# Performance work log

Hardware: AMD Instinct MI355X
Metric: run time of the kernel (lower is better)

## Reference

```python
import jax, jax.numpy as jnp
import numpy as np

EMBED = 512
HEADS = 8
INTER = 512
HEAD_DIM = INTER // HEADS
ROPE_BASE = 10000.0


def rot_half(x):
    x1 = x[..., ::2]
    x2 = x[..., 1::2]
    return jnp.stack([-x2, x1], axis=-1).reshape(x.shape)


def apply_rope(x, cos, sin):
    # cos/sin: (1, T, 1, 1, D//2) -> repeat-interleave to D
    cos = jnp.repeat(cos, 2, axis=-1)
    sin = jnp.repeat(sin, 2, axis=-1)
    return x * cos + rot_half(x) * sin


def setup_inputs() -> dict:
    key = jax.random.key(0)
    ks = jax.random.split(key, 8)
    B, T, P, E = 2, 512, 16, EMBED
    s_in = 1.0 / np.sqrt(E)
    x = jax.random.normal(ks[0], (B, T, P, E), dtype=jnp.float32)
    q_w = jax.random.normal(ks[1], (INTER, E), dtype=jnp.float32) * s_in
    k_w = jax.random.normal(ks[2], (INTER, E), dtype=jnp.float32) * s_in
    v_w = jax.random.normal(ks[3], (INTER, E), dtype=jnp.float32) * s_in
    q_b = jax.random.normal(ks[4], (INTER,), dtype=jnp.float32) * 0.01
    k_b = jax.random.normal(ks[5], (INTER,), dtype=jnp.float32) * 0.01
    v_b = jax.random.normal(ks[6], (INTER,), dtype=jnp.float32) * 0.01
    proj_w = jax.random.normal(ks[7], (E, INTER), dtype=jnp.float32) * (1.0 / np.sqrt(INTER))
    return {"x": x, "q_w": q_w, "q_b": q_b, "k_w": k_w, "k_b": k_b,
            "v_w": v_w, "v_b": v_b, "proj_w": proj_w}


def reference(x, q_w, q_b, k_w, k_b, v_w, v_b, proj_w):
    B, T, P, E = x.shape
    H, D = HEADS, HEAD_DIM
    q = (x @ q_w.T + q_b).reshape(B, T, P, H, D)
    k = (x @ k_w.T + k_b).reshape(B, T, P, H, D)
    v = (x @ v_w.T + v_b).reshape(B, T, P, H, D)
    # RoPE cache over time axis
    inv_freq = 1.0 / (ROPE_BASE ** (jnp.arange(0, D, 2, dtype=jnp.float32) / D))
    freqs = jnp.arange(T, dtype=jnp.float32)[:, None] * inv_freq[None, :]  # (T, D//2)
    cos_t = jnp.cos(freqs).reshape(1, T, 1, 1, D // 2)
    sin_t = jnp.sin(freqs).reshape(1, T, 1, 1, D // 2)
    q = apply_rope(q, cos_t, sin_t)
    k = apply_rope(k, cos_t, sin_t)
    scale = D ** (-0.5)
    scores = jnp.einsum('btphd,buphd->bphtu', q, k) * scale  # (B,P,H,T,T)
    causal_mask = jnp.triu(jnp.ones((T, T), dtype=bool), k=1)
    scores = jnp.where(causal_mask, -jnp.inf, scores)
    probs = jax.nn.softmax(scores, axis=-1)
    y = jnp.einsum('bphtu,buphd->btphd', probs, v).reshape(B, T, P, H * D)
    return y @ proj_w.T
```

## Files before the change

kernel.cpp:

```cpp
#include <hip/hip_runtime.h>
#include <hip/hip_bf16.h>
#include <math.h>

typedef __bf16 bf16x8 __attribute__((ext_vector_type(8)));
typedef float f32x4 __attribute__((ext_vector_type(4)));
typedef unsigned short u16;

#define MROWS 16384
#define TT 512
#define PP 16

__device__ __forceinline__ u16 f2bf(float f) {
    union { float f; unsigned int i; } v; v.f = f;
    unsigned int x = v.i;
    return (u16)((x + 0x7FFFu + ((x >> 16) & 1u)) >> 16);
}

__device__ __forceinline__ void async16(const u16* g, u16* lds) {
    __builtin_amdgcn_global_load_lds(
        (const __attribute__((address_space(1))) void*)g,
        (__attribute__((address_space(3))) void*)lds, 16, 0, 0);
}

__global__ __launch_bounds__(256) void cvt_k(const float* __restrict__ s,
                                             u16* __restrict__ d) {
    long i = (long)blockIdx.x * 256 + threadIdx.x;
    const float4* p = (const float4*)s + i * 2;
    float4 a = p[0], b = p[1];
    u16 t[8] = { f2bf(a.x), f2bf(a.y), f2bf(a.z), f2bf(a.w),
                 f2bf(b.x), f2bf(b.y), f2bf(b.z), f2bf(b.w) };
    *(uint4*)(d + i * 8) = *(const uint4*)t;
}

__global__ __launch_bounds__(256) void cvtw_k(const float* __restrict__ q,
                                              const float* __restrict__ k,
                                              const float* __restrict__ v,
                                              const float* __restrict__ pw,
                                              u16* __restrict__ d) {
    int m = blockIdx.y;
    const float* s = (m == 0) ? q : (m == 1) ? k : (m == 2) ? v : pw;
    long i = (long)blockIdx.x * 256 + threadIdx.x;
    const float4* p = (const float4*)s + i * 2;
    float4 a = p[0], b = p[1];
    u16 t[8] = { f2bf(a.x), f2bf(a.y), f2bf(a.z), f2bf(a.w),
                 f2bf(b.x), f2bf(b.y), f2bf(b.z), f2bf(b.w) };
    *(uint4*)(d + (long)m * 262144 + i * 8) = *(const uint4*)t;
}

template<bool QKV>
__global__ __launch_bounds__(256, 2)
void gemm_k(const u16* __restrict__ A, const u16* __restrict__ Wall,
            const float* __restrict__ bq, const float* __restrict__ bk,
            const float* __restrict__ bv,
            u16* __restrict__ Oq, u16* __restrict__ Ok, u16* __restrict__ Ov,
            float* __restrict__ Of)
{
    __shared__ u16 As[128 * 64];
    __shared__ u16 Bs[128 * 64];

    const int tid  = threadIdx.x;
    const int wv   = tid >> 6;
    const int lane = tid & 63;
    const int quad = lane >> 4;
    const int l16  = lane & 15;
    const int wm   = wv >> 1, wn = wv & 1;

    const int blockM = blockIdx.x;
    const int blockN = blockIdx.y;

    const u16* W; const float* bias; u16* OutB; int ncol0; int section = 0;
    if constexpr (QKV) {
        section = blockN >> 2;
        ncol0 = (blockN & 3) * 128;
        W    = Wall + (long)section * 262144;
        bias = (section == 0) ? bq : (section == 1) ? bk : bv;
        OutB = (section == 0) ? Oq : (section == 1) ? Ok : Ov;
    } else {
        ncol0 = blockN * 128;
        W = Wall; bias = nullptr; OutB = nullptr;
    }

    const int gm0 = blockM * 128;
    const int lr  = lane >> 3;
    const int lc  = (lane & 7) ^ lr;

    f32x4 acc[4][4] = {};

    for (int kk = 0; kk < 8; ++kk) {
        const int k0 = kk * 64;
        __syncthreads();
        #pragma unroll
        for (int i = 0; i < 4; ++i) {
            const int rb = wv * 32 + i * 8;
            async16(&A[(long)(gm0   + rb + lr) * 512 + k0 + lc * 8], &As[rb * 64]);
            async16(&W[(long)(ncol0 + rb + lr) * 512 + k0 + lc * 8], &Bs[rb * 64]);
        }
        __syncthreads();

        #pragma unroll
        for (int ks = 0; ks < 2; ++ks) {
            bf16x8 af[4], bf_[4];
            #pragma unroll
            for (int ms = 0; ms < 4; ++ms) {
                const int R = wm * 64 + ms * 16 + l16;
                af[ms] = *(const bf16x8*)&As[(R * 8 + ((ks * 4 + quad) ^ (l16 & 7))) * 8];
            }
            #pragma unroll
            for (int ns = 0; ns < 4; ++ns) {
                const int R = wn * 64 + ns * 16 + l16;
                bf_[ns] = *(const bf16x8*)&Bs[(R * 8 + ((ks * 4 + quad) ^ (l16 & 7))) * 8];
            }
            #pragma unroll
            for (int ms = 0; ms < 4; ++ms)
                #pragma unroll
                for (int ns = 0; ns < 4; ++ns)
                    acc[ms][ns] = __builtin_amdgcn_mfma_f32_16x16x32_bf16(af[ms], bf_[ns], acc[ms][ns], 0, 0, 0);
        }
    }

    #pragma unroll
    for (int ms = 0; ms < 4; ++ms) {
        const int g_m0 = gm0 + wm * 64 + ms * 16 + quad * 4;
        #pragma unroll
        for (int ns = 0; ns < 4; ++ns) {
            const int n_local = ncol0 + wn * 64 + ns * 16 + l16;
            float bval = 0.f;
            if constexpr (QKV) bval = bias[n_local];
            #pragma unroll
            for (int r = 0; r < 4; ++r) {
                float val = acc[ms][ns][r] + bval;
                const size_t off = (size_t)(g_m0 + r) * 512 + n_local;
                if constexpr (QKV) {
                    float partner = __shfl_xor(val, 1, 64);
                    if (section < 2) {
                        const int m = g_m0 + r;
                        const int t = (m >> 4) & 511;
                        const int d = n_local & 63;
                        float ang = (float)t * __expf(-(float)(d & ~1) * (9.210340371976184f / 64.0f));
                        float s_, c_;
                        __sincosf(ang, &s_, &c_);
                        val = (d & 1) ? (val * c_ + partner * s_)
                                      : (val * c_ - partner * s_);
                    }
                    OutB[off] = f2bf(val);
                } else {
                    Of[off] = val;
                }
            }
        }
    }
}

__global__ __launch_bounds__(256, 4)
void attn_k(const u16* __restrict__ Q, const u16* __restrict__ K,
            const u16* __restrict__ V, u16* __restrict__ Y)
{
    __shared__ u16 Sh[128][72];
    __shared__ u16 Vt[64][72];

    const int tid  = threadIdx.x;
    const int wv   = tid >> 6;
    const int lane = tid & 63;
    const int quad = lane >> 4;
    const int l16  = lane & 15;

    const int pairx = blockIdx.x;
    const int hid = blockIdx.y;
    const int b = hid >> 7;
    const int p = (hid >> 3) & 15;
    const int h = hid & 7;

    const int base = ((b * TT) * PP + p) * 512 + h * 64;
    const int rowStride = PP * 512;

    for (int sel = 0; sel < 2; ++sel) {
        const int qt = (sel == 0) ? pairx : 3 - pairx;
        const int t0 = qt * 128;

        __syncthreads();
        #pragma unroll
        for (int i = 0; i < 4; ++i) {
            int task = tid + i * 256;
            int row = task >> 3, c = (task & 7) * 8;
            *(uint4*)&Sh[row][c] = *(const uint4*)&Q[base + (t0 + row) * rowStride + c];
        }
        __syncthreads();
        bf16x8 qf[2][2];
        #pragma unroll
        for (int ms = 0; ms < 2; ++ms)
            #pragma unroll
            for (int ks = 0; ks < 2; ++ks)
                qf[ms][ks] = *(const bf16x8*)&Sh[wv*32 + ms*16 + l16][ks*32 + quad*8];

        float m_i[8], l_i[8], alpha[8];
        f32x4 o[2][4] = {};
        #pragma unroll
        for (int j = 0; j < 8; ++j) { m_i[j] = -3.0e38f; l_i[j] = 0.f; }

        const int nUT = (qt + 1) * 2;
        for (int ui = 0; ui < nUT; ++ui) {
            const int u0 = ui * 64;
            __syncthreads();
            #pragma unroll
            for (int i = 0; i < 2; ++i) {
                int task = tid + i * 256;
                int row = task >> 3, c = (task & 7) * 8;
                *(uint4*)&Sh[row][c] = *(const uint4*)&K[base + (u0 + row) * rowStride + c];
            }
            #pragma unroll
            for (int i = 0; i < 4; ++i) {
                int task = tid + i * 256;
                int u = task >> 4, dc = (task & 15) * 4;
                uint2 vvv = *(const uint2*)&V[base + (u0 + u) * rowStride + dc];
                Vt[dc + 0][u] = (u16)(vvv.x & 0xFFFF);
                Vt[dc + 1][u] = (u16)(vvv.x >> 16);
                Vt[dc + 2][u] = (u16)(vvv.y & 0xFFFF);
                Vt[dc + 3][u] = (u16)(vvv.y >> 16);
            }
            __syncthreads();

            f32x4 s[2][4] = {};
            #pragma unroll
            for (int ks = 0; ks < 2; ++ks) {
                bf16x8 bk_[4];
                #pragma unroll
                for (int ns = 0; ns < 4; ++ns)
                    bk_[ns] = *(const bf16x8*)&Sh[ns*16 + l16][ks*32 + quad*8];
                #pragma unroll
                for (int ms = 0; ms < 2; ++ms)
                    #pragma unroll
                    for (int ns = 0; ns < 4; ++ns)
                        s[ms][ns] = __builtin_amdgcn_mfma_f32_16x16x32_bf16(qf[ms][ks], bk_[ns], s[ms][ns], 0, 0, 0);
            }
            __syncthreads();

            #pragma unroll
            for (int ms = 0; ms < 2; ++ms)
                #pragma unroll
                for (int ns = 0; ns < 4; ++ns)
                    #pragma unroll
                    for (int r = 0; r < 4; ++r) {
                        int trow = t0 + wv*32 + ms*16 + quad*4 + r;
                        int ucol = u0 + ns*16 + l16;
                        float v = s[ms][ns][r] * 0.125f;
                        s[ms][ns][r] = (ucol > trow) ? -1.0e30f : v;
                    }
            #pragma unroll
            for (int ms = 0; ms < 2; ++ms) {
                #pragma unroll
                for (int r = 0; r < 4; ++r) {
                    const int j = ms*4 + r;
                    float tmax = s[ms][0][r];
                    #pragma unroll
                    for (int ns = 1; ns < 4; ++ns) tmax = fmaxf(tmax, s[ms][ns][r]);
                    #pragma unroll
                    for (int off = 1; off < 16; off <<= 1)
                        tmax = fmaxf(tmax, __shfl_xor(tmax, off, 64));
                    float mn = fmaxf(m_i[j], tmax);
                    alpha[j] = __expf(fminf(m_i[j] - mn, 0.f));
                    m_i[j] = mn;
                    float rsum = 0.f;
                    #pragma unroll
                    for (int ns = 0; ns < 4; ++ns) {
                        float e = __expf(fminf(s[ms][ns][r] - mn, 0.f));
                        s[ms][ns][r] = e;
                        rsum += e;
                    }
                    #pragma unroll
                    for (int off = 1; off < 16; off <<= 1)
                        rsum += __shfl_xor(rsum, off, 64);
                    l_i[j] = l_i[j] * alpha[j] + rsum;
                }
            }
            #pragma unroll
            for (int ms = 0; ms < 2; ++ms)
                #pragma unroll
                for (int nd = 0; nd < 4; ++nd)
                    #pragma unroll
                    for (int r = 0; r < 4; ++r)
                        o[ms][nd][r] *= alpha[ms*4 + r];
            #pragma unroll
            for (int ms = 0; ms < 2; ++ms)
                #pragma unroll
                for (int ns = 0; ns < 4; ++ns)
                    #pragma unroll
                    for (int r = 0; r < 4; ++r)
                        Sh[wv*32 + ms*16 + quad*4 + r][ns*16 + l16] = f2bf(s[ms][ns][r]);
            __syncthreads();
            #pragma unroll
            for (int ks = 0; ks < 2; ++ks) {
                bf16x8 ap[2], bv_[4];
                #pragma unroll
                for (int ms = 0; ms < 2; ++ms)
                    ap[ms] = *(const bf16x8*)&Sh[wv*32 + ms*16 + l16][ks*32 + quad*8];
                #pragma unroll
                for (int nd = 0; nd < 4; ++nd)
                    bv_[nd] = *(const bf16x8*)&Vt[nd*16 + l16][ks*32 + quad*8];
                #pragma unroll
                for (int ms = 0; ms < 2; ++ms)
                    #pragma unroll
                    for (int nd = 0; nd < 4; ++nd)
                        o[ms][nd] = __builtin_amdgcn_mfma_f32_16x16x32_bf16(ap[ms], bv_[nd], o[ms][nd], 0, 0, 0);
            }
        }

        #pragma unroll
        for (int ms = 0; ms < 2; ++ms)
            #pragma unroll
            for (int nd = 0; nd < 4; ++nd)
                #pragma unroll
                for (int r = 0; r < 4; ++r) {
                    int t = t0 + wv*32 + ms*16 + quad*4 + r;
                    int d = nd*16 + l16;
                    float val = o[ms][nd][r] / l_i[ms*4 + r];
                    int ym = (b * TT + t) * PP + p;
                    Y[ym * 512 + h * 64 + d] = f2bf(val);
                }
    }
}

extern "C" void kernel_launch(void* const* d_in, const int* in_sizes, int n_in,
                              void* d_out, int out_size, void* d_ws, size_t ws_size,
                              hipStream_t stream) {
    const float* x  = (const float*)d_in[0];
    const float* qw = (const float*)d_in[1];
    const float* qb = (const float*)d_in[2];
    const float* kw = (const float*)d_in[3];
    const float* kb = (const float*)d_in[4];
    const float* vw = (const float*)d_in[5];
    const float* vb = (const float*)d_in[6];
    const float* pw = (const float*)d_in[7];

    u16* ws   = (u16*)d_ws;
    u16* xb   = ws;
    u16* wAll = ws + (size_t)MROWS * 512;
    u16* Qb   = wAll + 4 * 262144;
    u16* Vb   = (u16*)d_out;
    u16* Kb   = (u16*)d_out + (size_t)MROWS * 512;

    cvt_k<<<4096, 256, 0, stream>>>(x, xb);
    cvtw_k<<<dim3(128, 4), 256, 0, stream>>>(qw, kw, vw, pw, wAll);
    gemm_k<true><<<dim3(128, 12), 256, 0, stream>>>(xb, wAll, qb, kb, vb,
                                                    Qb, Kb, Vb, nullptr);
    attn_k<<<dim3(2, 256), 256, 0, stream>>>(Qb, Kb, Vb, Qb);
    gemm_k<false><<<dim3(128, 4), 256, 0, stream>>>(Qb, wAll + 3 * 262144,
                                                    nullptr, nullptr, nullptr,
                                                    nullptr, nullptr, nullptr,
                                                    (float*)d_out);
}
```

Measured before the change: 227.7 us.

## Shrink attention query tile to 64 rows with swizzled async LDS loads

The attention kernel now handles 64-row query tiles instead of 128, pairing tiles (p, 7-p) so causal work stays balanced, and launches twice as many blocks. Q and K tiles go into an unpadded XOR-swizzled LDS buffer via async global-to-LDS loads, and the causal mask runs only on the diagonal tile. The aim is more parallelism and occupancy, less LDS, fewer masking ALU ops and no register staging for loads. In exchange each block reloads K/V more often relative to its MFMA work, since each wave now computes a single 16-row slice.

```diff
diff --git a/kernel.cpp b/kernel.cpp
--- a/kernel.cpp
+++ b/kernel.cpp
@@ -155,7 +155,7 @@
 void attn_k(const u16* __restrict__ Q, const u16* __restrict__ K,
             const u16* __restrict__ V, u16* __restrict__ Y)
 {
-    __shared__ u16 Sh[128][72];
+    __shared__ u16 Sh[64 * 64];
     __shared__ u16 Vt[64][72];
 
     const int tid  = threadIdx.x;
@@ -163,6 +163,8 @@
     const int lane = tid & 63;
     const int quad = lane >> 4;
     const int l16  = lane & 15;
+    const int lr   = lane >> 3;
+    const int lc   = (lane & 7) ^ lr;
 
     const int pairx = blockIdx.x;
     const int hid = blockIdx.y;
@@ -174,38 +176,36 @@
     const int rowStride = PP * 512;
 
     for (int sel = 0; sel < 2; ++sel) {
-        const int qt = (sel == 0) ? pairx : 3 - pairx;
-        const int t0 = qt * 128;
+        const int qt = sel ? (7 - pairx) : pairx;
+        const int t0 = qt * 64;
 
         __syncthreads();
         #pragma unroll
-        for (int i = 0; i < 4; ++i) {
-            int task = tid + i * 256;
-            int row = task >> 3, c = (task & 7) * 8;
-            *(uint4*)&Sh[row][c] = *(const uint4*)&Q[base + (t0 + row) * rowStride + c];
+        for (int i = 0; i < 2; ++i) {
+            const int rb = wv * 16 + i * 8;
+            async16(&Q[base + (t0 + rb + lr) * rowStride + lc * 8], &Sh[rb * 64]);
         }
         __syncthreads();
-        bf16x8 qf[2][2];
-        #pragma unroll
-        for (int ms = 0; ms < 2; ++ms)
+        bf16x8 qf[2];
+        {
+            const int R = wv * 16 + l16;
             #pragma unroll
             for (int ks = 0; ks < 2; ++ks)
-                qf[ms][ks] = *(const bf16x8*)&Sh[wv*32 + ms*16 + l16][ks*32 + quad*8];
-
-        float m_i[8], l_i[8], alpha[8];
-        f32x4 o[2][4] = {};
-        #pragma unroll
-        for (int j = 0; j < 8; ++j) { m_i[j] = -3.0e38f; l_i[j] = 0.f; }
-
-        const int nUT = (qt + 1) * 2;
-        for (int ui = 0; ui < nUT; ++ui) {
+                qf[ks] = *(const bf16x8*)&Sh[(R * 8 + ((ks * 4 + quad) ^ (l16 & 7))) * 8];
+        }
+
+        float m_i[4], l_i[4], alpha[4];
+        f32x4 o[4] = {};
+        #pragma unroll
+        for (int j = 0; j < 4; ++j) { m_i[j] = -3.0e38f; l_i[j] = 0.f; }
+
+        for (int ui = 0; ui <= qt; ++ui) {
             const int u0 = ui * 64;
             __syncthreads();
             #pragma unroll
             for (int i = 0; i < 2; ++i) {
-                int task = tid + i * 256;
-                int row = task >> 3, c = (task & 7) * 8;
-                *(uint4*)&Sh[row][c] = *(const uint4*)&K[base + (u0 + row) * rowStride + c];
+                const int rb = wv * 16 + i * 8;
+                async16(&K[base + (u0 + rb + lr) * rowStride + lc * 8], &Sh[rb * 64]);
             }
             #pragma unroll
             for (int i = 0; i < 4; ++i) {
@@ -219,103 +219,99 @@
             }
             __syncthreads();
 
-            f32x4 s[2][4] = {};
+            f32x4 s[4] = {};
             #pragma unroll
             for (int ks = 0; ks < 2; ++ks) {
                 bf16x8 bk_[4];
                 #pragma unroll
+                for (int ns = 0; ns < 4; ++ns) {
+                    const int R = ns * 16 + l16;
+                    bk_[ns] = *(const bf16x8*)&Sh[(R * 8 + ((ks * 4 + quad) ^ (l16 & 7))) * 8];
+                }
+                #pragma unroll
                 for (int ns = 0; ns < 4; ++ns)
-                    bk_[ns] = *(const bf16x8*)&Sh[ns*16 + l16][ks*32 + quad*8];
-                #pragma unroll
-                for (int ms = 0; ms < 2; ++ms)
-                    #pragma unroll
-                    for (int ns = 0; ns < 4; ++ns)
-                        s[ms][ns] = __builtin_amdgcn_mfma_f32_16x16x32_bf16(qf[ms][ks], bk_[ns], s[ms][ns], 0, 0, 0);
+                    s[ns] = __builtin_amdgcn_mfma_f32_16x16x32_bf16(qf[ks], bk_[ns], s[ns], 0, 0, 0);
             }
             __syncthreads();
 
-            #pragma unroll
-            for (int ms = 0; ms < 2; ++ms)
+            if (ui == qt) {
                 #pragma unroll
                 for (int ns = 0; ns < 4; ++ns)
                     #pragma unroll
                     for (int r = 0; r < 4; ++r) {
-                        int trow = t0 + wv*32 + ms*16 + quad*4 + r;
-                        int ucol = u0 + ns*16 + l16;
-                        float v = s[ms][ns][r] * 0.125f;
-                        s[ms][ns][r] = (ucol > trow) ? -1.0e30f : v;
+                        int trow = wv * 16 + quad * 4 + r;
+                        int ucol = ns * 16 + l16;
+                        float v = s[ns][r] * 0.125f;
+                        s[ns][r] = (ucol > trow) ? -1.0e30f : v;
                     }
-            #pragma unroll
-            for (int ms = 0; ms < 2; ++ms) {
-                #pragma unroll
-                for (int r = 0; r < 4; ++r) {
-                    const int j = ms*4 + r;
-                    float tmax = s[ms][0][r];
-                    #pragma unroll
-                    for (int ns = 1; ns < 4; ++ns) tmax = fmaxf(tmax, s[ms][ns][r]);
-                    #pragma unroll
-                    for (int off = 1; off < 16; off <<= 1)
-                        tmax = fmaxf(tmax, __shfl_xor(tmax, off, 64));
-                    float mn = fmaxf(m_i[j], tmax);
-                    alpha[j] = __expf(fminf(m_i[j] - mn, 0.f));
-                    m_i[j] = mn;
-                    float rsum = 0.f;
-                    #pragma unroll
-                    for (int ns = 0; ns < 4; ++ns) {
-                        float e = __expf(fminf(s[ms][ns][r] - mn, 0.f));
-                        s[ms][ns][r] = e;
-                        rsum += e;
-                    }
-                    #pragma unroll
-                    for (int off = 1; off < 16; off <<= 1)
-                        rsum += __shfl_xor(rsum, off, 64);
-                    l_i[j] = l_i[j] * alpha[j] + rsum;
-                }
-            }
-            #pragma unroll
-            for (int ms = 0; ms < 2; ++ms)
-                #pragma unroll
-                for (int nd = 0; nd < 4; ++nd)
-                    #pragma unroll
-                    for (int r = 0; r < 4; ++r)
-                        o[ms][nd][r] *= alpha[ms*4 + r];
-            #pragma unroll
-            for (int ms = 0; ms < 2; ++ms)
+            } else {
                 #pragma unroll
                 for (int ns = 0; ns < 4; ++ns)
                     #pragma unroll
                     for (int r = 0; r < 4; ++r)
-                        Sh[wv*32 + ms*16 + quad*4 + r][ns*16 + l16] = f2bf(s[ms][ns][r]);
+                        s[ns][r] *= 0.125f;
+            }
+            #pragma unroll
+            for (int r = 0; r < 4; ++r) {
+                float tmax = s[0][r];
+                #pragma unroll
+                for (int ns = 1; ns < 4; ++ns) tmax = fmaxf(tmax, s[ns][r]);
+                #pragma unroll
+                for (int off = 1; off < 16; off <<= 1)
+                    tmax = fmaxf(tmax, __shfl_xor(tmax, off, 64));
+                float mn = fmaxf(m_i[r], tmax);
+                alpha[r] = __expf(fminf(m_i[r] - mn, 0.f));
+                m_i[r] = mn;
+                float rsum = 0.f;
+                #pragma unroll
+                for (int ns = 0; ns < 4; ++ns) {
+                    float e = __expf(fminf(s[ns][r] - mn, 0.f));
+                    s[ns][r] = e;
+                    rsum += e;
+                }
+                #pragma unroll
+                for (int off = 1; off < 16; off <<= 1)
+                    rsum += __shfl_xor(rsum, off, 64);
+                l_i[r] = l_i[r] * alpha[r] + rsum;
+            }
+            #pragma unroll
+            for (int nd = 0; nd < 4; ++nd)
+                #pragma unroll
+                for (int r = 0; r < 4; ++r)
+                    o[nd][r] *= alpha[r];
+            #pragma unroll
+            for (int ns = 0; ns < 4; ++ns)
+                #pragma unroll
+                for (int r = 0; r < 4; ++r) {
+                    const int row = wv * 16 + quad * 4 + r;
+                    const int cu  = ns * 2 + (l16 >> 3);
+                    Sh[(row * 8 + (cu ^ (row & 7))) * 8 + (l16 & 7)] = f2bf(s[ns][r]);
+                }
             __syncthreads();
             #pragma unroll
             for (int ks = 0; ks < 2; ++ks) {
-                bf16x8 ap[2], bv_[4];
-                #pragma unroll
-                for (int ms = 0; ms < 2; ++ms)
-                    ap[ms] = *(const bf16x8*)&Sh[wv*32 + ms*16 + l16][ks*32 + quad*8];
+                const int R = wv * 16 + l16;
+                bf16x8 ap = *(const bf16x8*)&Sh[(R * 8 + ((ks * 4 + quad) ^ (l16 & 7))) * 8];
+                bf16x8 bv_[4];
                 #pragma unroll
                 for (int nd = 0; nd < 4; ++nd)
-                    bv_[nd] = *(const bf16x8*)&Vt[nd*16 + l16][ks*32 + quad*8];
-                #pragma unroll
-                for (int ms = 0; ms < 2; ++ms)
-                    #pragma unroll
-                    for (int nd = 0; nd < 4; ++nd)
-                        o[ms][nd] = __builtin_amdgcn_mfma_f32_16x16x32_bf16(ap[ms], bv_[nd], o[ms][nd], 0, 0, 0);
-            }
-        }
-
-        #pragma unroll
-        for (int ms = 0; ms < 2; ++ms)
-            #pragma unroll
-            for (int nd = 0; nd < 4; ++nd)
-                #pragma unroll
-                for (int r = 0; r < 4; ++r) {
-                    int t = t0 + wv*32 + ms*16 + quad*4 + r;
-                    int d = nd*16 + l16;
-                    float val = o[ms][nd][r] / l_i[ms*4 + r];
-                    int ym = (b * TT + t) * PP + p;
-                    Y[ym * 512 + h * 64 + d] = f2bf(val);
-                }
+                    bv_[nd] = *(const bf16x8*)&Vt[nd * 16 + l16][ks * 32 + quad * 8];
+                #pragma unroll
+                for (int nd = 0; nd < 4; ++nd)
+                    o[nd] = __builtin_amdgcn_mfma_f32_16x16x32_bf16(ap, bv_[nd], o[nd], 0, 0, 0);
+            }
+        }
+
+        #pragma unroll
+        for (int nd = 0; nd < 4; ++nd)
+            #pragma unroll
+            for (int r = 0; r < 4; ++r) {
+                int t = t0 + wv * 16 + quad * 4 + r;
+                int d = nd * 16 + l16;
+                float val = o[nd][r] / l_i[r];
+                int ym = (b * TT + t) * PP + p;
+                Y[ym * 512 + h * 64 + d] = f2bf(val);
+            }
     }
 }
 
@@ -342,7 +338,7 @@
     cvtw_k<<<dim3(128, 4), 256, 0, stream>>>(qw, kw, vw, pw, wAll);
     gemm_k<true><<<dim3(128, 12), 256, 0, stream>>>(xb, wAll, qb, kb, vb,
                                                     Qb, Kb, Vb, nullptr);
-    attn_k<<<dim3(2, 256), 256, 0, stream>>>(Qb, Kb, Vb, Qb);
+    attn_k<<<dim3(4, 256), 256, 0, stream>>>(Qb, Kb, Vb, Qb);
     gemm_k<false><<<dim3(128, 4), 256, 0, stream>>>(Qb, wAll + 3 * 262144,
                                                     nullptr, nullptr, nullptr,
                                                     nullptr, nullptr, nullptr,
```

Result: faster. 195.9 us (-14.0%).
